# Optimization experiments

Measured on AMD Instinct MI355X. Metric: run time of the kernel, lower is better.

## Reference

```python
import jax, jax.numpy as jnp
import numpy as np

N = 50000
IN_C, HID_C, CLS_C = 512, 256, 128
E = 800000


def setup_inputs() -> dict:
    key = jax.random.key(0)
    k1, k2, k3, k4, k5, k6 = jax.random.split(key, 6)
    x = jax.random.normal(k1, (N, IN_C), dtype=jnp.float32)
    edge_index = jax.random.randint(k2, (2, E), 0, N, dtype=jnp.int64)
    # GCNConv params (glorot weights, zero bias as in PyG init)
    W1 = jax.random.normal(k3, (IN_C, HID_C), dtype=jnp.float32) * (1.0 / np.sqrt(IN_C))
    b1 = jnp.zeros((HID_C,), dtype=jnp.float32)
    W2 = jax.random.normal(k4, (HID_C, CLS_C), dtype=jnp.float32) * (1.0 / np.sqrt(HID_C))
    b2 = jnp.zeros((CLS_C,), dtype=jnp.float32)
    return {"x": x, "W1": W1, "b1": b1, "W2": W2, "b2": b2, "edge_index": edge_index}


def _norm_edges(edge_index, n):
    # PyG GCNConv: add self-loops, symmetric normalization deg^-1/2
    loops = jnp.arange(n, dtype=edge_index.dtype)
    src = jnp.concatenate([edge_index[0], loops])
    dst = jnp.concatenate([edge_index[1], loops])
    ones = jnp.ones_like(src, dtype=jnp.float32)
    deg = jax.ops.segment_sum(ones, dst, num_segments=n)
    dinv = jnp.where(deg > 0, jax.lax.rsqrt(deg), 0.0)
    norm = dinv[src] * dinv[dst]  # [E+N]
    return src, dst, norm


def _gcn_conv(x, W, b, src, dst, norm, n):
    h = x @ W  # project first (out_channels < in_channels)
    msg = h[src] * norm[:, None]  # gather + scale, [E+N, C]
    out = jax.ops.segment_sum(msg, dst, num_segments=n)  # scatter-add
    return out + b


def reference(x, W1, b1, W2, b2, edge_index):
    n = x.shape[0]
    src, dst, norm = _norm_edges(edge_index, n)
    h = jax.nn.relu(_gcn_conv(x, W1, b1, src, dst, norm, n))
    # dropout p=0.5 is a no-op in eval mode
    out = _gcn_conv(h, W2, b2, src, dst, norm, n)
    return jax.nn.sigmoid(out)
```

## Files before the change

### kernel.cpp

```cpp
#include <hip/hip_runtime.h>

typedef __attribute__((ext_vector_type(8))) short bf16x8;
typedef __attribute__((ext_vector_type(4))) float f32x4;
typedef unsigned short u16;
typedef unsigned int u32;
typedef __attribute__((address_space(1))) const u32 gu32;
typedef __attribute__((address_space(3))) u32 lu32;

__device__ __forceinline__ float bf2f(u16 u) {
  union { u32 i; float f; } c; c.i = ((u32)u) << 16; return c.f;
}
__device__ __forceinline__ u16 f2bf(float f) {
  union { float f; u32 i; } c; c.f = f;
  u32 u = c.i;
  u32 r = (u + 0x7FFFu + ((u >> 16) & 1u)) >> 16;
  return (u16)r;
}

__device__ __forceinline__ void gld16(const void* g, void* l) {
  __builtin_amdgcn_global_load_lds((gu32*)g, (lu32*)l, 16, 0, 0);
}


__global__ void k_count(const int* __restrict__ ei, int* deg, int E) {
  int e = blockIdx.x * 256 + threadIdx.x;
  if (e < E) atomicAdd(&deg[ei[E + e]], 1);
}

__global__ void k_blocksum(const int* __restrict__ deg, int* bsum, int n) {
  __shared__ int s[256];
  int t = threadIdx.x;
  int i = blockIdx.x * 256 + t;
  s[t] = (i < n) ? deg[i] : 0;
  __syncthreads();
  for (int o = 128; o > 0; o >>= 1) {
    if (t < o) s[t] += s[t + o];
    __syncthreads();
  }
  if (t == 0) bsum[blockIdx.x] = s[0];
}

__global__ void k_scanb(const int* __restrict__ bsum, int* bofs, int nb) {
  __shared__ int s[256];
  int t = threadIdx.x;
  int v = (t < nb) ? bsum[t] : 0;
  s[t] = v;
  __syncthreads();
  for (int o = 1; o < 256; o <<= 1) {
    int x = (t >= o) ? s[t - o] : 0;
    __syncthreads();
    s[t] += x;
    __syncthreads();
  }
  bofs[t] = s[t] - v;
}

__global__ void k_rowptr(const int* __restrict__ deg, const int* __restrict__ bofs,
                         int* rowptr, int* cursor, float* dinv, int n) {
  __shared__ int s[256];
  int t = threadIdx.x;
  int i = blockIdx.x * 256 + t;
  int v = (i < n) ? deg[i] : 0;
  s[t] = v;
  __syncthreads();
  for (int o = 1; o < 256; o <<= 1) {
    int x = (t >= o) ? s[t - o] : 0;
    __syncthreads();
    s[t] += x;
    __syncthreads();
  }
  int excl = s[t] - v + bofs[blockIdx.x];
  if (i < n) {
    rowptr[i] = excl;
    cursor[i] = excl;
    dinv[i] = rsqrtf((float)(v + 1));
    if (i == n - 1) rowptr[n] = excl + v;
  }
}

__global__ void k_fill(const int* __restrict__ ei, int* cursor,
                       const float* __restrict__ dinv, int2* colw, int E) {
  int e = blockIdx.x * 256 + threadIdx.x;
  if (e >= E) return;
  int s = ei[e];
  int d = ei[E + e];
  int pos = atomicAdd(&cursor[d], 1);
  colw[pos] = make_int2(s, __float_as_int(dinv[s]));
}

__global__ void k_twt2(const float* __restrict__ W1, u16* __restrict__ W1t,
                       const float* __restrict__ W2, u16* __restrict__ W2t) {
  int i = blockIdx.x * 256 + threadIdx.x;
  if (i < 512 * 256) {
    int k = i >> 8, n = i & 255;
    W1t[n * 512 + k] = f2bf(W1[i]);
  } else {
    int j = i - 512 * 256;
    if (j < 256 * 128) {
      int k = j >> 7, n = j & 127;
      W2t[n * 256 + k] = f2bf(W2[j]);
    }
  }
}


template <bool AF32, int K, int COLS>
__launch_bounds__(1024)
__global__ void gemm3(const void* __restrict__ Ap, const u16* __restrict__ Bt,
                      u16* __restrict__ C, int M, int ldc) {
  constexpr int NT = K / 32;
  constexpr int SLABU = COLS * 4;
  constexpr int NB = (COLS * K / 8) / 1024;
  constexpr int NJ = COLS / 16;
  __shared__ __align__(16) u16 Bs[NT][COLS * 32];

  const int tid = threadIdx.x;
  const int lane = tid & 63;
  const int w = tid >> 6;
  const long brow = (long)blockIdx.y * 256;
  const long bcol = (long)blockIdx.x * COLS;

#pragma unroll
  for (int j = 0; j < NB; ++j) {
    int g = j * 1024 + tid;
    int kt = g / SLABU;
    int s = g - kt * SLABU;
    int c = s >> 2;
    int u = (s & 3) ^ (c & 3);
    gld16(Bt + (bcol + c) * (long)K + kt * 32 + u * 8,
          (char*)&Bs[0][0] + (size_t)g * 16);
  }
  __syncthreads();

  long arow = brow + w * 16 + (lane & 15);
  if (arow > (long)M - 1) arow = M - 1;
  const char* ap = (const char*)Ap + (arow * (long)K + (lane >> 4) * 8) * (AF32 ? 4 : 2);
  constexpr int AST = 32 * (AF32 ? 4 : 2);

  f32x4 acc[NJ];
#pragma unroll
  for (int j = 0; j < NJ; ++j) acc[j] = (f32x4){0.f, 0.f, 0.f, 0.f};

  float4 fa[2][2];
  uint4 fb[2];
  auto loadA = [&](int kt, int sl) {
    if constexpr (AF32) {
      fa[sl][0] = *(const float4*)(ap + (size_t)kt * AST);
      fa[sl][1] = *(const float4*)(ap + (size_t)kt * AST + 16);
    } else {
      fb[sl] = *(const uint4*)(ap + (size_t)kt * AST);
    }
  };
  loadA(0, 0);
  loadA(1, 1);

#pragma unroll
  for (int kt = 0; kt < NT; ++kt) {
    const int sl = kt & 1;
    bf16x8 af;
    if constexpr (AF32) {
      union { u32 wd[4]; bf16x8 v; } cv;
      asm("v_cvt_pk_bf16_f32 %0, %1, %2" : "=v"(cv.wd[0]) : "v"(fa[sl][0].x), "v"(fa[sl][0].y));
      asm("v_cvt_pk_bf16_f32 %0, %1, %2" : "=v"(cv.wd[1]) : "v"(fa[sl][0].z), "v"(fa[sl][0].w));
      asm("v_cvt_pk_bf16_f32 %0, %1, %2" : "=v"(cv.wd[2]) : "v"(fa[sl][1].x), "v"(fa[sl][1].y));
      asm("v_cvt_pk_bf16_f32 %0, %1, %2" : "=v"(cv.wd[3]) : "v"(fa[sl][1].z), "v"(fa[sl][1].w));
      af = cv.v;
    } else {
      union { uint4 q; bf16x8 v; } cv2;
      cv2.q = fb[sl];
      af = cv2.v;
    }
    if (kt + 2 < NT) loadA(kt + 2, sl);
#pragma unroll
    for (int j = 0; j < NJ; ++j) {
      const int row = j * 16 + (lane & 15);
      const int u = (lane >> 4) ^ (row & 3);
      bf16x8 bq = *(const bf16x8*)&Bs[kt][row * 32 + u * 8];
      acc[j] = __builtin_amdgcn_mfma_f32_16x16x32_bf16(af, bq, acc[j], 0, 0, 0);
    }
  }

#pragma unroll
  for (int j = 0; j < NJ; ++j) {
    const long cc = bcol + j * 16 + (lane & 15);
    const long r0 = brow + w * 16 + ((lane >> 4) * 4);
#pragma unroll
    for (int q = 0; q < 4; ++q) {
      long r = r0 + q;
      if (r < M) C[r * (long)ldc + cc] = f2bf(acc[j][q]);
    }
  }
}


__device__ __forceinline__ float sigmoidf_(float x) { return 1.f / (1.f + __expf(-x)); }

__launch_bounds__(256)
__global__ void agg1(const u16* __restrict__ h0, const int* __restrict__ rowptr,
                     const int2* __restrict__ colw, const float* __restrict__ dinv,
                     const float* __restrict__ b1, u16* __restrict__ h, int n) {
  const int wid = threadIdx.x >> 6, lane = threadIdx.x & 63;
  const int node = blockIdx.x * 4 + wid;
  if (node >= n) return;
  const float di = dinv[node];
  ushort4 sv = ((const ushort4*)(h0 + (size_t)node * 256))[lane];
  float a0 = di * bf2f(sv.x), a1 = di * bf2f(sv.y), a2 = di * bf2f(sv.z), a3 = di * bf2f(sv.w);
  int e = rowptr[node];
  const int r1 = rowptr[node + 1];
  for (; e + 8 <= r1; e += 8) {
    int2 c[8];
#pragma unroll
    for (int q = 0; q < 8; ++q) c[q] = colw[e + q];
    ushort4 v[8];
#pragma unroll
    for (int q = 0; q < 8; ++q)
      v[q] = ((const ushort4*)(h0 + (size_t)c[q].x * 256))[lane];
#pragma unroll
    for (int q = 0; q < 8; ++q) {
      float wv = __int_as_float(c[q].y);
      a0 += wv * bf2f(v[q].x); a1 += wv * bf2f(v[q].y);
      a2 += wv * bf2f(v[q].z); a3 += wv * bf2f(v[q].w);
    }
  }
  for (; e < r1; ++e) {
    int2 c = colw[e];
    float wv = __int_as_float(c.y);
    ushort4 v = ((const ushort4*)(h0 + (size_t)c.x * 256))[lane];
    a0 += wv * bf2f(v.x); a1 += wv * bf2f(v.y); a2 += wv * bf2f(v.z); a3 += wv * bf2f(v.w);
  }
  float4 bb = ((const float4*)b1)[lane];
  a0 = a0 * di + bb.x; a1 = a1 * di + bb.y; a2 = a2 * di + bb.z; a3 = a3 * di + bb.w;
  a0 = fmaxf(a0, 0.f); a1 = fmaxf(a1, 0.f); a2 = fmaxf(a2, 0.f); a3 = fmaxf(a3, 0.f);
  ushort4 o; o.x = f2bf(a0); o.y = f2bf(a1); o.z = f2bf(a2); o.w = f2bf(a3);
  ((ushort4*)(h + (size_t)node * 256))[lane] = o;
}

__launch_bounds__(256)
__global__ void agg2(const u16* __restrict__ h2, const int* __restrict__ rowptr,
                     const int2* __restrict__ colw, const float* __restrict__ dinv,
                     const float* __restrict__ b2, float* __restrict__ out, int n) {
  const int wid = threadIdx.x >> 6, lane = threadIdx.x & 63;
  const int node = blockIdx.x * 4 + wid;
  if (node >= n) return;
  const float di = dinv[node];
  ushort2 sv = ((const ushort2*)(h2 + (size_t)node * 128))[lane];
  float a0 = di * bf2f(sv.x), a1 = di * bf2f(sv.y);
  int e = rowptr[node];
  const int r1 = rowptr[node + 1];
  for (; e + 8 <= r1; e += 8) {
    int2 c[8];
#pragma unroll
    for (int q = 0; q < 8; ++q) c[q] = colw[e + q];
    ushort2 v[8];
#pragma unroll
    for (int q = 0; q < 8; ++q)
      v[q] = ((const ushort2*)(h2 + (size_t)c[q].x * 128))[lane];
#pragma unroll
    for (int q = 0; q < 8; ++q) {
      float wv = __int_as_float(c[q].y);
      a0 += wv * bf2f(v[q].x); a1 += wv * bf2f(v[q].y);
    }
  }
  for (; e < r1; ++e) {
    int2 c = colw[e];
    float wv = __int_as_float(c.y);
    ushort2 v = ((const ushort2*)(h2 + (size_t)c.x * 128))[lane];
    a0 += wv * bf2f(v.x); a1 += wv * bf2f(v.y);
  }
  float2 bb = ((const float2*)b2)[lane];
  float2 o;
  o.x = sigmoidf_(a0 * di + bb.x);
  o.y = sigmoidf_(a1 * di + bb.y);
  ((float2*)(out + (size_t)node * 128))[lane] = o;
}


extern "C" void kernel_launch(void* const* d_in, const int* in_sizes, int n_in,
                              void* d_out, int out_size, void* d_ws, size_t ws_size,
                              hipStream_t stream) {
  const float* x  = (const float*)d_in[0];
  const float* W1 = (const float*)d_in[1];
  const float* b1 = (const float*)d_in[2];
  const float* W2 = (const float*)d_in[3];
  const float* b2 = (const float*)d_in[4];
  const int*   ei = (const int*)d_in[5];

  const int N = in_sizes[0] / 512;
  const int E = in_sizes[5] / 2;
  const int Mpad = (N + 127) & ~127;
  float* outp = (float*)d_out;

  char* w = (char*)d_ws;
  size_t off = 0;
  auto take = [&](size_t bytes) -> void* {
    void* p = w + off;
    off = (off + bytes + 255) & ~(size_t)255;
    return p;
  };
  u16*   h0     = (u16*)take((size_t)Mpad * 256 * 2);
  u16*   hb     = (u16*)take((size_t)Mpad * 256 * 2);
  u16*   h2     = (u16*)take((size_t)Mpad * 128 * 2);
  u16*   W1t    = (u16*)take(256 * 512 * 2);
  u16*   W2t    = (u16*)take(128 * 256 * 2);
  int*   deg    = (int*)take((size_t)N * 4);
  float* dinv   = (float*)take((size_t)N * 4);
  int*   rowptr = (int*)take((size_t)(N + 1) * 4);
  int*   cursor = (int*)take((size_t)N * 4);
  int2*  colw   = (int2*)take((size_t)E * 8);
  int*   bsum   = (int*)take(256 * 4);
  int*   bofs   = (int*)take(256 * 4);
  (void)ws_size; (void)n_in; (void)out_size;

  const int nb = (N + 255) / 256;
  const int eb = (E + 255) / 256;

  hipMemsetAsync(deg, 0, (size_t)N * 4, stream);
  k_count<<<eb, 256, 0, stream>>>(ei, deg, E);
  k_blocksum<<<nb, 256, 0, stream>>>(deg, bsum, N);
  k_scanb<<<1, 256, 0, stream>>>(bsum, bofs, nb);
  k_rowptr<<<nb, 256, 0, stream>>>(deg, bofs, rowptr, cursor, dinv, N);
  k_fill<<<eb, 256, 0, stream>>>(ei, cursor, dinv, colw, E);
  k_twt2<<<(512 * 256 + 256 * 128 + 255) / 256, 256, 0, stream>>>(W1, W1t, W2, W2t);

  const int rb = (N + 255) / 256;
  dim3 g1(2, rb);
  gemm3<true, 512, 128><<<g1, 1024, 0, stream>>>((const void*)x, W1t, h0, N, 256);
  agg1<<<(N + 3) / 4, 256, 0, stream>>>(h0, rowptr, colw, dinv, b1, hb, N);
  dim3 g2(1, rb);
  gemm3<false, 256, 128><<<g2, 1024, 0, stream>>>((const void*)hb, W2t, h2, N, 128);
  agg2<<<(N + 3) / 4, 256, 0, stream>>>(h2, rowptr, colw, dinv, b2, outp, N);
}
```

Measured before the change: 253.8 us.

## Keep A tile in registers and loop over both column tiles per block

The first GEMM previously launched two blocks per row tile, so each read the fp32 x rows and converted them to bf16 separately. Now one block loads and converts its full A strip into registers once, then computes both 128-column halves in turn, restaging B in LDS between them. The second B slab load is placed alongside the first tile's output writes. This halves global reads of x, but costs many more VGPRs per thread (an A strip of 16 bf16x8 vectors plus accumulators), halves the grid, and serialises the two column tiles inside one block.

```diff
diff --git a/kernel.cpp b/kernel.cpp
--- a/kernel.cpp
+++ b/kernel.cpp
@@ -104,91 +104,108 @@
 }
 
 
-template <bool AF32, int K, int COLS>
+template <bool AF32, int K, int CT>
 __launch_bounds__(1024)
-__global__ void gemm3(const void* __restrict__ Ap, const u16* __restrict__ Bt,
+__global__ void gemm4(const void* __restrict__ Ap, const u16* __restrict__ Bt,
                       u16* __restrict__ C, int M, int ldc) {
   constexpr int NT = K / 32;
-  constexpr int SLABU = COLS * 4;
-  constexpr int NB = (COLS * K / 8) / 1024;
-  constexpr int NJ = COLS / 16;
-  __shared__ __align__(16) u16 Bs[NT][COLS * 32];
+  constexpr int NB = NT / 2;
+  __shared__ __align__(16) u16 Bs[NT][4096];
 
   const int tid = threadIdx.x;
   const int lane = tid & 63;
   const int w = tid >> 6;
-  const long brow = (long)blockIdx.y * 256;
-  const long bcol = (long)blockIdx.x * COLS;
-
-#pragma unroll
-  for (int j = 0; j < NB; ++j) {
-    int g = j * 1024 + tid;
-    int kt = g / SLABU;
-    int s = g - kt * SLABU;
-    int c = s >> 2;
-    int u = (s & 3) ^ (c & 3);
-    gld16(Bt + (bcol + c) * (long)K + kt * 32 + u * 8,
-          (char*)&Bs[0][0] + (size_t)g * 16);
-  }
-  __syncthreads();
+  const long brow = (long)blockIdx.x * 256;
 
   long arow = brow + w * 16 + (lane & 15);
   if (arow > (long)M - 1) arow = M - 1;
   const char* ap = (const char*)Ap + (arow * (long)K + (lane >> 4) * 8) * (AF32 ? 4 : 2);
-  constexpr int AST = 32 * (AF32 ? 4 : 2);
-
-  f32x4 acc[NJ];
-#pragma unroll
-  for (int j = 0; j < NJ; ++j) acc[j] = (f32x4){0.f, 0.f, 0.f, 0.f};
-
-  float4 fa[2][2];
-  uint4 fb[2];
-  auto loadA = [&](int kt, int sl) {
-    if constexpr (AF32) {
-      fa[sl][0] = *(const float4*)(ap + (size_t)kt * AST);
-      fa[sl][1] = *(const float4*)(ap + (size_t)kt * AST + 16);
-    } else {
-      fb[sl] = *(const uint4*)(ap + (size_t)kt * AST);
+
+  auto stage = [&](int ct) {
+    const long bcol = (long)ct * 128;
+#pragma unroll
+    for (int j = 0; j < NB; ++j) {
+      int g = j * 1024 + tid;
+      int kt = g >> 9;
+      int s = g & 511;
+      int c = s >> 2;
+      int u = (s & 3) ^ (c & 3);
+      gld16(Bt + (bcol + c) * (long)K + kt * 32 + u * 8,
+            (char*)&Bs[0][0] + (size_t)g * 16);
     }
   };
-  loadA(0, 0);
-  loadA(1, 1);
-
-#pragma unroll
-  for (int kt = 0; kt < NT; ++kt) {
-    const int sl = kt & 1;
-    bf16x8 af;
-    if constexpr (AF32) {
-      union { u32 wd[4]; bf16x8 v; } cv;
-      asm("v_cvt_pk_bf16_f32 %0, %1, %2" : "=v"(cv.wd[0]) : "v"(fa[sl][0].x), "v"(fa[sl][0].y));
-      asm("v_cvt_pk_bf16_f32 %0, %1, %2" : "=v"(cv.wd[1]) : "v"(fa[sl][0].z), "v"(fa[sl][0].w));
-      asm("v_cvt_pk_bf16_f32 %0, %1, %2" : "=v"(cv.wd[2]) : "v"(fa[sl][1].x), "v"(fa[sl][1].y));
-      asm("v_cvt_pk_bf16_f32 %0, %1, %2" : "=v"(cv.wd[3]) : "v"(fa[sl][1].z), "v"(fa[sl][1].w));
-      af = cv.v;
-    } else {
-      union { uint4 q; bf16x8 v; } cv2;
-      cv2.q = fb[sl];
-      af = cv2.v;
-    }
-    if (kt + 2 < NT) loadA(kt + 2, sl);
-#pragma unroll
-    for (int j = 0; j < NJ; ++j) {
-      const int row = j * 16 + (lane & 15);
-      const int u = (lane >> 4) ^ (row & 3);
-      bf16x8 bq = *(const bf16x8*)&Bs[kt][row * 32 + u * 8];
-      acc[j] = __builtin_amdgcn_mfma_f32_16x16x32_bf16(af, bq, acc[j], 0, 0, 0);
-    }
-  }
-
-#pragma unroll
-  for (int j = 0; j < NJ; ++j) {
-    const long cc = bcol + j * 16 + (lane & 15);
-    const long r0 = brow + w * 16 + ((lane >> 4) * 4);
-#pragma unroll
-    for (int q = 0; q < 4; ++q) {
-      long r = r0 + q;
-      if (r < M) C[r * (long)ldc + cc] = f2bf(acc[j][q]);
-    }
+
+  stage(0);
+
+  bf16x8 areg[NT];
+  if constexpr (AF32) {
+#pragma unroll
+    for (int g = 0; g < NT; g += 4) {
+      float4 t[8];
+#pragma unroll
+      for (int q = 0; q < 4; ++q) {
+        t[2 * q] = *(const float4*)(ap + (size_t)(g + q) * 128);
+        t[2 * q + 1] = *(const float4*)(ap + (size_t)(g + q) * 128 + 16);
+      }
+#pragma unroll
+      for (int q = 0; q < 4; ++q) {
+        union { u32 wd[4]; bf16x8 v; } cv;
+        asm("v_cvt_pk_bf16_f32 %0, %1, %2" : "=v"(cv.wd[0]) : "v"(t[2*q].x), "v"(t[2*q].y));
+        asm("v_cvt_pk_bf16_f32 %0, %1, %2" : "=v"(cv.wd[1]) : "v"(t[2*q].z), "v"(t[2*q].w));
+        asm("v_cvt_pk_bf16_f32 %0, %1, %2" : "=v"(cv.wd[2]) : "v"(t[2*q+1].x), "v"(t[2*q+1].y));
+        asm("v_cvt_pk_bf16_f32 %0, %1, %2" : "=v"(cv.wd[3]) : "v"(t[2*q+1].z), "v"(t[2*q+1].w));
+        areg[g + q] = cv.v;
+      }
+    }
+  } else {
+#pragma unroll
+    for (int kt = 0; kt < NT; ++kt) {
+      union { uint4 q; bf16x8 v; } cv;
+      cv.q = *(const uint4*)(ap + (size_t)kt * 64);
+      areg[kt] = cv.v;
+    }
+  }
+
+  f32x4 acc[8];
+  auto compute = [&]() {
+#pragma unroll
+    for (int j = 0; j < 8; ++j) acc[j] = (f32x4){0.f, 0.f, 0.f, 0.f};
+#pragma unroll
+    for (int kt = 0; kt < NT; ++kt) {
+#pragma unroll
+      for (int j = 0; j < 8; ++j) {
+        const int c = j * 16 + (lane & 15);
+        const int u = (lane >> 4) ^ (c & 3);
+        bf16x8 bq = *(const bf16x8*)&Bs[kt][c * 32 + u * 8];
+        acc[j] = __builtin_amdgcn_mfma_f32_16x16x32_bf16(areg[kt], bq, acc[j], 0, 0, 0);
+      }
+    }
+  };
+  auto writeC = [&](int ct) {
+    const long bcol = (long)ct * 128;
+#pragma unroll
+    for (int j = 0; j < 8; ++j) {
+      const long cc = bcol + j * 16 + (lane & 15);
+      const long r0 = brow + w * 16 + ((lane >> 4) * 4);
+#pragma unroll
+      for (int q = 0; q < 4; ++q) {
+        long r = r0 + q;
+        if (r < M) C[r * (long)ldc + cc] = f2bf(acc[j][q]);
+      }
+    }
+  };
+
+  __syncthreads();
+  compute();
+  if constexpr (CT == 2) {
+    __syncthreads();
+    stage(1);
+    writeC(0);
+    __syncthreads();
+    compute();
+    writeC(1);
+  } else {
+    writeC(0);
   }
 }
 
@@ -323,10 +340,8 @@
   k_twt2<<<(512 * 256 + 256 * 128 + 255) / 256, 256, 0, stream>>>(W1, W1t, W2, W2t);
 
   const int rb = (N + 255) / 256;
-  dim3 g1(2, rb);
-  gemm3<true, 512, 128><<<g1, 1024, 0, stream>>>((const void*)x, W1t, h0, N, 256);
+  gemm4<true, 512, 2><<<rb, 1024, 0, stream>>>((const void*)x, W1t, h0, N, 256);
   agg1<<<(N + 3) / 4, 256, 0, stream>>>(h0, rowptr, colw, dinv, b1, hb, N);
-  dim3 g2(1, rb);
-  gemm3<false, 256, 128><<<g2, 1024, 0, stream>>>((const void*)hb, W2t, h2, N, 128);
+  gemm4<false, 256, 1><<<rb, 1024, 0, stream>>>((const void*)hb, W2t, h2, N, 128);
   agg2<<<(N + 3) / 4, 256, 0, stream>>>(h2, rowptr, colw, dinv, b2, outp, N);
 }
```

New measurement: 274.0 us. 1.08x slower.

## Replace LDS-staged GEMM with register-only GEMM reading B directly from global

Applied to the files above, without the earlier changes.

The projection GEMMs no longer stage the transposed weight matrix in shared memory with a block-wide barrier. Each wave instead loads B fragments straight from global memory (relying on L1/L2 caching) and computes all output columns for 16 rows. Blocks shrink from 1024 to 256 threads with 64 rows each, which raises the block count and occupancy hint. The cost is repeated global/cache traffic for B per wave, and large per-thread accumulator arrays (16 fragments) that add register pressure.

```diff
diff --git a/kernel.cpp b/kernel.cpp
--- a/kernel.cpp
+++ b/kernel.cpp
@@ -4,8 +4,6 @@
 typedef __attribute__((ext_vector_type(4))) float f32x4;
 typedef unsigned short u16;
 typedef unsigned int u32;
-typedef __attribute__((address_space(1))) const u32 gu32;
-typedef __attribute__((address_space(3))) u32 lu32;
 
 __device__ __forceinline__ float bf2f(u16 u) {
   union { u32 i; float f; } c; c.i = ((u32)u) << 16; return c.f;
@@ -15,10 +13,6 @@
   u32 u = c.i;
   u32 r = (u + 0x7FFFu + ((u >> 16) & 1u)) >> 16;
   return (u16)r;
-}
-
-__device__ __forceinline__ void gld16(const void* g, void* l) {
-  __builtin_amdgcn_global_load_lds((gu32*)g, (lu32*)l, 16, 0, 0);
 }
 
 
@@ -104,55 +98,37 @@
 }
 
 
-template <bool AF32, int K, int COLS>
-__launch_bounds__(1024)
-__global__ void gemm3(const void* __restrict__ Ap, const u16* __restrict__ Bt,
+template <bool AF32, int K, int NJ>
+__launch_bounds__(256, 4)
+__global__ void gemm5(const void* __restrict__ Ap, const u16* __restrict__ Bt,
                       u16* __restrict__ C, int M, int ldc) {
   constexpr int NT = K / 32;
-  constexpr int SLABU = COLS * 4;
-  constexpr int NB = (COLS * K / 8) / 1024;
-  constexpr int NJ = COLS / 16;
-  __shared__ __align__(16) u16 Bs[NT][COLS * 32];
-
   const int tid = threadIdx.x;
   const int lane = tid & 63;
   const int w = tid >> 6;
-  const long brow = (long)blockIdx.y * 256;
-  const long bcol = (long)blockIdx.x * COLS;
-
-#pragma unroll
-  for (int j = 0; j < NB; ++j) {
-    int g = j * 1024 + tid;
-    int kt = g / SLABU;
-    int s = g - kt * SLABU;
-    int c = s >> 2;
-    int u = (s & 3) ^ (c & 3);
-    gld16(Bt + (bcol + c) * (long)K + kt * 32 + u * 8,
-          (char*)&Bs[0][0] + (size_t)g * 16);
-  }
-  __syncthreads();
-
-  long arow = brow + w * 16 + (lane & 15);
+  const long row0 = (long)blockIdx.x * 64 + w * 16;
+
+  long arow = row0 + (lane & 15);
   if (arow > (long)M - 1) arow = M - 1;
   const char* ap = (const char*)Ap + (arow * (long)K + (lane >> 4) * 8) * (AF32 ? 4 : 2);
-  constexpr int AST = 32 * (AF32 ? 4 : 2);
+  const u16* bp = Bt + ((long)(lane & 15) * K + (lane >> 4) * 8);
 
   f32x4 acc[NJ];
 #pragma unroll
   for (int j = 0; j < NJ; ++j) acc[j] = (f32x4){0.f, 0.f, 0.f, 0.f};
 
   float4 fa[2][2];
-  uint4 fb[2];
+  uint4 fh[2];
   auto loadA = [&](int kt, int sl) {
     if constexpr (AF32) {
-      fa[sl][0] = *(const float4*)(ap + (size_t)kt * AST);
-      fa[sl][1] = *(const float4*)(ap + (size_t)kt * AST + 16);
+      fa[sl][0] = *(const float4*)(ap + (size_t)kt * 128);
+      fa[sl][1] = *(const float4*)(ap + (size_t)kt * 128 + 16);
     } else {
-      fb[sl] = *(const uint4*)(ap + (size_t)kt * AST);
+      fh[sl] = *(const uint4*)(ap + (size_t)kt * 64);
     }
   };
   loadA(0, 0);
-  loadA(1, 1);
+  if (NT > 1) loadA(1, 1);
 
 #pragma unroll
   for (int kt = 0; kt < NT; ++kt) {
@@ -167,23 +143,22 @@
       af = cv.v;
     } else {
       union { uint4 q; bf16x8 v; } cv2;
-      cv2.q = fb[sl];
+      cv2.q = fh[sl];
       af = cv2.v;
     }
     if (kt + 2 < NT) loadA(kt + 2, sl);
 #pragma unroll
     for (int j = 0; j < NJ; ++j) {
-      const int row = j * 16 + (lane & 15);
-      const int u = (lane >> 4) ^ (row & 3);
-      bf16x8 bq = *(const bf16x8*)&Bs[kt][row * 32 + u * 8];
-      acc[j] = __builtin_amdgcn_mfma_f32_16x16x32_bf16(af, bq, acc[j], 0, 0, 0);
+      union { uint4 q; bf16x8 v; } bq;
+      bq.q = *(const uint4*)(bp + (size_t)j * 16 * K + (size_t)kt * 32);
+      acc[j] = __builtin_amdgcn_mfma_f32_16x16x32_bf16(af, bq.v, acc[j], 0, 0, 0);
     }
   }
 
 #pragma unroll
   for (int j = 0; j < NJ; ++j) {
-    const long cc = bcol + j * 16 + (lane & 15);
-    const long r0 = brow + w * 16 + ((lane >> 4) * 4);
+    const long cc = j * 16 + (lane & 15);
+    const long r0 = row0 + ((lane >> 4) * 4);
 #pragma unroll
     for (int q = 0; q < 4; ++q) {
       long r = r0 + q;
@@ -322,11 +297,9 @@
   k_fill<<<eb, 256, 0, stream>>>(ei, cursor, dinv, colw, E);
   k_twt2<<<(512 * 256 + 256 * 128 + 255) / 256, 256, 0, stream>>>(W1, W1t, W2, W2t);
 
-  const int rb = (N + 255) / 256;
-  dim3 g1(2, rb);
-  gemm3<true, 512, 128><<<g1, 1024, 0, stream>>>((const void*)x, W1t, h0, N, 256);
+  const int gb = (N + 63) / 64;
+  gemm5<true, 512, 16><<<gb, 256, 0, stream>>>((const void*)x, W1t, h0, N, 256);
   agg1<<<(N + 3) / 4, 256, 0, stream>>>(h0, rowptr, colw, dinv, b1, hb, N);
-  dim3 g2(1, rb);
-  gemm3<false, 256, 128><<<g2, 1024, 0, stream>>>((const void*)hb, W2t, h2, N, 128);
+  gemm5<false, 256, 8><<<gb, 256, 0, stream>>>((const void*)hb, W2t, h2, N, 128);
   agg2<<<(N + 3) / 4, 256, 0, stream>>>(h2, rowptr, colw, dinv, b2, outp, N);
 }
```

After: 372.0 us. +46.6%, slower.
